# Kernel tuning notes

Hardware: AMD Instinct MI355X
Metric: run time of the kernel (lower is better)

Reference implementation:

```python
import jax, jax.numpy as jnp
import numpy as np

N_GROUPS = 32
EPS = 1e-5
N_HEADS = 4
D_K = 64


def group_norm(x, gamma, beta):
    # x: [B, C, H, W]; normalize over (channels within group, spatial)
    B, C, H, W = x.shape
    xg = x.reshape(B, N_GROUPS, C // N_GROUPS, H, W)
    mean = jnp.mean(xg, axis=(2, 3, 4), keepdims=True)
    var = jnp.var(xg, axis=(2, 3, 4), keepdims=True)
    xn = ((xg - mean) * jax.lax.rsqrt(var + EPS)).reshape(B, C, H, W)
    return xn * gamma[None, :, None, None] + beta[None, :, None, None]


def setup_inputs() -> dict:
    key = jax.random.key(0)
    ks = jax.random.split(key, 4)
    B, C, H, W = 4, 256, 64, 64
    x = jax.random.normal(ks[0], (B, C, H, W), dtype=jnp.float32)
    gamma = jnp.ones((C,), dtype=jnp.float32)
    beta = jnp.zeros((C,), dtype=jnp.float32)
    w_qkv = jax.random.normal(ks[1], (C, N_HEADS * D_K * 3), dtype=jnp.float32) * (C ** -0.5)
    b_qkv = jnp.zeros((N_HEADS * D_K * 3,), dtype=jnp.float32)
    w_out = jax.random.normal(ks[2], (N_HEADS * D_K, C), dtype=jnp.float32) * ((N_HEADS * D_K) ** -0.5)
    b_out = jnp.zeros((C,), dtype=jnp.float32)
    return {"x": x, "gamma": gamma, "beta": beta, "w_qkv": w_qkv,
            "b_qkv": b_qkv, "w_out": w_out, "b_out": b_out}


def reference(x, gamma, beta, w_qkv, b_qkv, w_out, b_out):
    B, C, H, W = x.shape
    S = H * W
    scale = D_K ** -0.5
    # GroupNorm -> [B, S, C]
    h = group_norm(x, gamma, beta).reshape(B, C, S).transpose(0, 2, 1)
    qkv = (h @ w_qkv + b_qkv).reshape(B, S, N_HEADS, 3 * D_K)
    q, k, v = jnp.split(qkv, 3, axis=-1)          # each [B, S, H, D]
    attn = jnp.einsum('bihd,bjhd->bijh', q, k) * scale
    attn = jax.nn.softmax(attn, axis=2)           # softmax over j (keys)
    res = jnp.einsum('bijh,bjhd->bihd', attn, v)  # [B, S, H, D]
    res = res.reshape(B, S, N_HEADS * D_K)
    res = res @ w_out + b_out                     # [B, S, C]
    res = res.transpose(0, 2, 1).reshape(B, C, H, W)
    return res + x
```

## Files before the change

kernel.cpp:

```cpp
#include <hip/hip_runtime.h>
#include <hip/hip_bf16.h>


typedef __attribute__((ext_vector_type(8))) short short8;
typedef __attribute__((ext_vector_type(4))) float f32x4;
typedef __attribute__((ext_vector_type(16))) float f32x16;

__device__ __forceinline__ unsigned short f2bf(float f) {
    union { float f; unsigned u; } v; v.f = f;
    unsigned r = v.u + 0x7FFF + ((v.u >> 16) & 1);
    return (unsigned short)(r >> 16);
}

__device__ __forceinline__ unsigned cvt_pk_bf16(float lo, float hi) {
    unsigned r;
    asm("v_cvt_pk_bf16_f32 %0, %1, %2" : "=v"(r) : "v"(lo), "v"(hi));
    return r;
}

__device__ __forceinline__ void permswap(unsigned &x, unsigned &y) {
    asm("v_permlane32_swap_b32 %0, %1" : "+v"(x), "+v"(y));
}

__device__ __forceinline__ float fexp2(float x) {
    float r;
    asm("v_exp_f32 %0, %1" : "=v"(r) : "v"(x));
    return r;
}

__device__ __forceinline__ void gl_lds16(const void* g, void* l) {
    __builtin_amdgcn_global_load_lds(
        (const __attribute__((address_space(1))) void*)(g),
        (__attribute__((address_space(3))) void*)(l), 16, 0, 0);
}

__device__ __forceinline__ f32x16 fzero16() {
    f32x16 z;
    #pragma unroll
    for (int i = 0; i < 16; ++i) z[i] = 0.f;
    return z;
}

__global__ __launch_bounds__(1024) void k_pre(
    const float* __restrict__ x, float* __restrict__ stats,
    const float* __restrict__ wqkv, const float* __restrict__ wout,
    unsigned short* __restrict__ wqkvT, unsigned short* __restrict__ woutT) {
    if (blockIdx.x < 128) {
        int bg = blockIdx.x;
        const float4* xp = (const float4*)(x + bg * 32768);
        float s1 = 0.f, s2 = 0.f;
        for (int i = threadIdx.x; i < 8192; i += 1024) {
            float4 v = xp[i];
            s1 += v.x + v.y + v.z + v.w;
            s2 += v.x*v.x + v.y*v.y + v.z*v.z + v.w*v.w;
        }
        #pragma unroll
        for (int off = 32; off; off >>= 1) {
            s1 += __shfl_down(s1, off);
            s2 += __shfl_down(s2, off);
        }
        __shared__ float r1[16], r2[16];
        int wid = threadIdx.x >> 6;
        if ((threadIdx.x & 63) == 0) { r1[wid] = s1; r2[wid] = s2; }
        __syncthreads();
        if (threadIdx.x == 0) {
            float a = 0.f, b = 0.f;
            #pragma unroll
            for (int i = 0; i < 16; ++i) { a += r1[i]; b += r2[i]; }
            float mean = a * (1.f/32768.f);
            float var  = b * (1.f/32768.f) - mean*mean;
            stats[bg*2]   = mean;
            stats[bg*2+1] = rsqrtf(var + 1e-5f);
        }
    } else {
        int i = (blockIdx.x - 128) * 1024 + threadIdx.x;
        if (i < 196608) {
            int k = i / 768, n = i - k * 768;
            wqkvT[n*256 + k] = f2bf(wqkv[i]);
        }
        if (i < 65536) {
            int k = i >> 8, n = i & 255;
            woutT[n*256 + k] = f2bf(wout[i]);
        }
    }
}

__global__ __launch_bounds__(512, 2) void k_qkvf(
    const float* __restrict__ x, const float* __restrict__ gamma,
    const float* __restrict__ beta, const float* __restrict__ stats,
    const unsigned short* __restrict__ wT, const float* __restrict__ bqkv,
    unsigned short* __restrict__ q, unsigned short* __restrict__ kk,
    unsigned short* __restrict__ vT) {
    __shared__ unsigned short t[64][72];
    __shared__ unsigned short lds_h[64][272];

    int m0 = blockIdx.x * 64;
    int b = m0 >> 12;
    int s0 = m0 & 4095;
    int tid = threadIdx.x;

    #pragma unroll
    for (int cb = 0; cb < 4; ++cb) {
        int c0 = cb * 64;
        #pragma unroll
        for (int k = 0; k < 2; ++k) {
            int u = tid + k * 512;
            int cr = u >> 4;
            int sl = (u & 15) * 4;
            int c = c0 + cr;
            float4 v = *(const float4*)&x[(b*256 + c)*4096 + s0 + sl];
            int sg = (b*32 + (c >> 3)) * 2;
            float mean = stats[sg], rstd = stats[sg+1];
            float sa = rstd * gamma[c];
            float sb = beta[c] - mean * sa;
            ushort4 pk;
            pk.x = f2bf(v.x*sa + sb); pk.y = f2bf(v.y*sa + sb);
            pk.z = f2bf(v.z*sa + sb); pk.w = f2bf(v.w*sa + sb);
            *(ushort4*)&t[cr][sl] = pk;
        }
        __syncthreads();
        int sr = tid >> 3;
        int cc8 = (tid & 7) * 8;
        unsigned rr[4];
        #pragma unroll
        for (int j = 0; j < 4; ++j)
            rr[j] = (unsigned)t[cc8 + 2*j][sr] | ((unsigned)t[cc8 + 2*j + 1][sr] << 16);
        *(uint4*)&lds_h[sr][c0 + cc8] = make_uint4(rr[0], rr[1], rr[2], rr[3]);
        __syncthreads();
    }

    int wid = tid >> 6, lane = tid & 63;
    int g = lane >> 4, li = lane & 15;
    int rg = wid & 3, cg = wid >> 2;
    int rowl = rg * 16 + li;
    f32x4 acc[24];
    #pragma unroll
    for (int nt = 0; nt < 24; ++nt) acc[nt] = (f32x4){0.f,0.f,0.f,0.f};
    #pragma unroll
    for (int kt = 0; kt < 8; ++kt) {
        short8 a = *(const short8*)&lds_h[rowl][kt*32 + g*8];
        #pragma unroll
        for (int nt = 0; nt < 24; ++nt) {
            int n = cg*384 + nt*16 + li;
            short8 bb = *(const short8*)&wT[n*256 + kt*32 + g*8];
            acc[nt] = __builtin_amdgcn_mfma_f32_16x16x32_bf16(a, bb, acc[nt], 0, 0, 0);
        }
    }
    int m0w = m0 + rg * 16;
    int s0w = m0w & 4095;
    #pragma unroll
    for (int nt = 0; nt < 24; ++nt) {
        int ng = cg*384 + nt*16 + li;
        int head = cg*2 + nt/12;
        int ntl = nt % 12;
        int bh = b*4 + head;
        float bias = bqkv[ng];
        int d = (ntl & 3)*16 + li;
        if ((ntl >> 2) == 2) {
            ushort4 pk;
            pk.x = f2bf(acc[nt][0] + bias); pk.y = f2bf(acc[nt][1] + bias);
            pk.z = f2bf(acc[nt][2] + bias); pk.w = f2bf(acc[nt][3] + bias);
            *(ushort4*)&vT[(bh*64 + d)*4096 + s0w + g*4] = pk;
        } else if ((ntl >> 2) == 0) {
            #pragma unroll
            for (int r = 0; r < 4; ++r)
                q[(bh*4096 + s0w + g*4 + r)*64 + d] = f2bf((acc[nt][r] + bias) * 0.1803368801f);
        } else {
            #pragma unroll
            for (int r = 0; r < 4; ++r)
                kk[(bh*4096 + s0w + g*4 + r)*64 + d] = f2bf(acc[nt][r] + bias);
        }
    }
}

__global__ __launch_bounds__(512, 4) void k_attn(
    const unsigned short* __restrict__ q, const unsigned short* __restrict__ kk,
    const unsigned short* __restrict__ vT, unsigned short* __restrict__ ao) {
    __shared__ __align__(16) char smem[65536];

    int n = blockIdx.x;
    int qt = n >> 4;
    int bh = ((n & 7) << 1) | ((n >> 3) & 1);
    int tid = threadIdx.x;
    int wid = tid >> 6, lane = tid & 63;
    int qw = wid & 3, st = wid >> 2;
    int hi = lane >> 5, il = lane & 31;
    int swl = (il & 7) << 4;

    int qbase = qt * 128 + qw * 32;
    int qrow = bh * 4096 + qbase + il;
    short8 bq[4];
    #pragma unroll
    for (int kc = 0; kc < 4; ++kc)
        bq[kc] = *(const short8*)&q[qrow*64 + kc*16 + hi*8];

    short8 ones;
    #pragma unroll
    for (int i = 0; i < 8; ++i) ones[i] = (short)0x3F80;

    unsigned p16  = tid * 16;
    unsigned row0 = p16 >> 7;
    unsigned sw   = (row0 & 7) << 4;
    unsigned ks0  = p16 ^ sw;
    unsigned vc0  = (p16 & 127u) ^ sw;
    const char* kbase = (const char*)kk + (size_t)bh * 524288;
    const char* vbase = (const char*)vT + (size_t)(bh*64 + row0) * 8192;
    unsigned woff = wid * 1024;

#define STAGE_PAIR(d, pair) do {                                             \
    const char* _k0 = kbase + (size_t)(2*(pair)) * 8192;                     \
    size_t _vo = (size_t)(2*(pair)) * 128;                                   \
    gl_lds16(_k0 + ks0,              smem + ((d)*2+0)*8192 + woff);          \
    gl_lds16(_k0 + 8192 + ks0,       smem + ((d)*2+1)*8192 + woff);          \
    gl_lds16(vbase + _vo + vc0,       smem + 32768 + ((d)*2+0)*8192 + woff); \
    gl_lds16(vbase + _vo + 128 + vc0, smem + 32768 + ((d)*2+1)*8192 + woff); \
} while (0)

    f32x16 o0 = fzero16(), o1 = fzero16(), accl = fzero16();
    float m_run = 0.f;

    STAGE_PAIR(0, 0);
    asm volatile("s_waitcnt vmcnt(0)" ::: "memory");
    __builtin_amdgcn_s_barrier();
    asm volatile("" ::: "memory");

    int cur = 0;
    for (int tp = 0; tp < 32; ++tp) {
        if (tp < 31) STAGE_PAIR(cur ^ 1, tp + 1);

        const char* kb = smem + (cur*2 + st) * 8192;
        const char* vb = smem + 32768 + (cur*2 + st) * 8192;

        float nm = -m_run;
        f32x16 p0, p1;
        #pragma unroll
        for (int r = 0; r < 16; ++r) { p0[r] = nm; p1[r] = nm; }
        __builtin_amdgcn_s_setprio(1);
        #pragma unroll
        for (int kc = 0; kc < 4; ++kc) {
            int c = (kc*32 + hi*16) ^ swl;
            short8 ka0 = *(const short8*)(kb + il*128 + c);
            short8 ka1 = *(const short8*)(kb + 4096 + il*128 + c);
            p0 = __builtin_amdgcn_mfma_f32_32x32x16_bf16(ka0, bq[kc], p0, 0, 0, 0);
            p1 = __builtin_amdgcn_mfma_f32_32x32x16_bf16(ka1, bq[kc], p1, 0, 0, 0);
        }
        __builtin_amdgcn_s_setprio(0);

        #pragma unroll
        for (int r = 0; r < 16; ++r) {
            p0[r] = fexp2(p0[r]);
            p1[r] = fexp2(p1[r]);
        }
        float m8[8];
        #pragma unroll
        for (int r = 0; r < 8; ++r)
            m8[r] = fmaxf(fmaxf(p0[2*r], p0[2*r+1]), fmaxf(p1[2*r], p1[2*r+1]));
        float pm = fmaxf(fmaxf(fmaxf(m8[0], m8[1]), fmaxf(m8[2], m8[3])),
                         fmaxf(fmaxf(m8[4], m8[5]), fmaxf(m8[6], m8[7])));
        if (__any(pm > 16.f)) {
            pm = fmaxf(pm, __shfl_xor(pm, 32));
            float fac = 1.f / pm;
            m_run += log2f(pm);
            accl[0] *= fac;
            #pragma unroll
            for (int r = 0; r < 16; ++r) {
                o0[r] *= fac; o1[r] *= fac;
                p0[r] *= fac; p1[r] *= fac;
            }
        }

        __builtin_amdgcn_s_setprio(1);
        #pragma unroll
        for (int jc = 0; jc < 4; ++jc) {
            const int hh = jc & 1;
            float e0, e1, e2, e3, e4, e5, e6, e7;
            if (jc < 2) {
                e0 = p0[hh*8+0]; e1 = p0[hh*8+1]; e2 = p0[hh*8+2]; e3 = p0[hh*8+3];
                e4 = p0[hh*8+4]; e5 = p0[hh*8+5]; e6 = p0[hh*8+6]; e7 = p0[hh*8+7];
            } else {
                e0 = p1[hh*8+0]; e1 = p1[hh*8+1]; e2 = p1[hh*8+2]; e3 = p1[hh*8+3];
                e4 = p1[hh*8+4]; e5 = p1[hh*8+5]; e6 = p1[hh*8+6]; e7 = p1[hh*8+7];
            }
            unsigned a = cvt_pk_bf16(e0, e1);
            unsigned b = cvt_pk_bf16(e2, e3);
            unsigned c = cvt_pk_bf16(e4, e5);
            unsigned d = cvt_pk_bf16(e6, e7);
            permswap(a, c);
            permswap(b, d);
            union { unsigned u[4]; short8 s8; } pb;
            pb.u[0] = a; pb.u[1] = b; pb.u[2] = c; pb.u[3] = d;
            int co = (jc*32 + hi*16) ^ swl;
            short8 va0 = *(const short8*)(vb + il*128 + co);
            short8 va1 = *(const short8*)(vb + 4096 + il*128 + co);
            o0   = __builtin_amdgcn_mfma_f32_32x32x16_bf16(va0, pb.s8, o0, 0, 0, 0);
            o1   = __builtin_amdgcn_mfma_f32_32x32x16_bf16(va1, pb.s8, o1, 0, 0, 0);
            accl = __builtin_amdgcn_mfma_f32_32x32x16_bf16(ones, pb.s8, accl, 0, 0, 0);
        }
        __builtin_amdgcn_s_setprio(0);

        if (tp < 31) asm volatile("s_waitcnt vmcnt(0)" ::: "memory");
        asm volatile("" ::: "memory");
        __builtin_amdgcn_s_barrier();
        asm volatile("" ::: "memory");
        cur ^= 1;
    }
#undef STAGE_PAIR

    float l_loc = accl[0];

    float* red = (float*)smem;
    int slot = ((qw*64 + lane) * 34);
    if (st == 1) {
        #pragma unroll
        for (int r = 0; r < 16; ++r) { red[slot + r] = o0[r]; red[slot + 16 + r] = o1[r]; }
        red[slot + 32] = l_loc;
        red[slot + 33] = m_run;
    }
    __syncthreads();
    if (st == 0) {
        float m1 = red[slot + 33], l1 = red[slot + 32];
        float m = fmaxf(m_run, m1);
        float f0 = fexp2(m_run - m), f1 = fexp2(m1 - m);
        float inv = 1.f / (l_loc * f0 + l1 * f1);
        float a0 = f0 * inv, a1 = f1 * inv;
        int b = bh >> 2, hh = bh & 3;
        int s = qbase + il;
        unsigned short* aop = &ao[((size_t)(b*4096 + s))*256 + hh*64];
        #pragma unroll
        for (int rr = 0; rr < 4; ++rr) {
            ushort4 pk0, pk1;
            pk0.x = f2bf(o0[rr*4+0]*a0 + red[slot + rr*4+0]*a1);
            pk0.y = f2bf(o0[rr*4+1]*a0 + red[slot + rr*4+1]*a1);
            pk0.z = f2bf(o0[rr*4+2]*a0 + red[slot + rr*4+2]*a1);
            pk0.w = f2bf(o0[rr*4+3]*a0 + red[slot + rr*4+3]*a1);
            *(ushort4*)&aop[rr*8 + hi*4] = pk0;
            pk1.x = f2bf(o1[rr*4+0]*a0 + red[slot + 16 + rr*4+0]*a1);
            pk1.y = f2bf(o1[rr*4+1]*a0 + red[slot + 16 + rr*4+1]*a1);
            pk1.z = f2bf(o1[rr*4+2]*a0 + red[slot + 16 + rr*4+2]*a1);
            pk1.w = f2bf(o1[rr*4+3]*a0 + red[slot + 16 + rr*4+3]*a1);
            *(ushort4*)&aop[32 + rr*8 + hi*4] = pk1;
        }
    }
}

__global__ __launch_bounds__(256) void k_out(
    const unsigned short* __restrict__ ao, const unsigned short* __restrict__ wT,
    const float* __restrict__ bout, const float* __restrict__ x,
    float* __restrict__ out) {
    int mt = blockIdx.x;
    int tid = threadIdx.x;
    int wid = tid >> 6, lane = tid & 63;
    int g = lane >> 4, li = lane & 15;
    int rg = wid & 1, ch = wid >> 1;
    int m0 = mt * 32 + rg * 16;
    int row = m0 + li;
    f32x4 acc[8];
    #pragma unroll
    for (int nt = 0; nt < 8; ++nt) acc[nt] = (f32x4){0.f,0.f,0.f,0.f};
    #pragma unroll
    for (int kt = 0; kt < 8; ++kt) {
        short8 a = *(const short8*)&ao[row*256 + kt*32 + g*8];
        #pragma unroll
        for (int nt = 0; nt < 8; ++nt) {
            int nn = ch*128 + nt*16 + li;
            short8 b = *(const short8*)&wT[nn*256 + kt*32 + g*8];
            acc[nt] = __builtin_amdgcn_mfma_f32_16x16x32_bf16(a, b, acc[nt], 0, 0, 0);
        }
    }
    int b = m0 >> 12;
    int s0 = (m0 & 4095) + g*4;
    #pragma unroll
    for (int nt = 0; nt < 8; ++nt) {
        int c = ch*128 + nt*16 + li;
        float bias = bout[c];
        int base = (b*256 + c)*4096 + s0;
        float4 xr = *(const float4*)&x[base];
        float4 ov;
        ov.x = acc[nt][0] + bias + xr.x;
        ov.y = acc[nt][1] + bias + xr.y;
        ov.z = acc[nt][2] + bias + xr.z;
        ov.w = acc[nt][3] + bias + xr.w;
        *(float4*)&out[base] = ov;
    }
}

extern "C" void kernel_launch(void* const* d_in, const int* in_sizes, int n_in,
                              void* d_out, int out_size, void* d_ws, size_t ws_size,
                              hipStream_t stream) {
    (void)in_sizes; (void)n_in; (void)out_size; (void)ws_size;
    const float* x     = (const float*)d_in[0];
    const float* gamma = (const float*)d_in[1];
    const float* beta  = (const float*)d_in[2];
    const float* wqkv  = (const float*)d_in[3];
    const float* bqkv  = (const float*)d_in[4];
    const float* wout  = (const float*)d_in[5];
    const float* bout  = (const float*)d_in[6];
    float* out = (float*)d_out;

    char* ws = (char*)d_ws;
    unsigned short* q     = (unsigned short*)(ws + (8u<<20));
    unsigned short* kk    = (unsigned short*)(ws + (16u<<20));
    unsigned short* vT    = (unsigned short*)(ws + (24u<<20));
    unsigned short* ao    = (unsigned short*)(ws + (32u<<20));
    unsigned short* wqkvT = (unsigned short*)(ws + (40u<<20));
    unsigned short* woutT = (unsigned short*)(ws + (40u<<20) + 393216);
    float*          stats = (float*)(ws + (40u<<20) + 524288);

    k_pre<<<320, 1024, 0, stream>>>(x, stats, wqkv, wout, wqkvT, woutT);
    k_qkvf<<<256, 512, 0, stream>>>(x, gamma, beta, stats, wqkvT, bqkv, q, kk, vT);
    k_attn<<<dim3(512), 512, 0, stream>>>(q, kk, vT, ao);
    k_out<<<dim3(512), 256, 0, stream>>>(ao, woutT, bout, x, out);
}
```

Before: 170.4 us.

## Retile QKV GEMM warps and stage output-projection tile through LDS for coalesced stores

```diff
diff --git a/kernel.cpp b/kernel.cpp
--- a/kernel.cpp
+++ b/kernel.cpp
@@ -131,44 +131,47 @@
 
     int wid = tid >> 6, lane = tid & 63;
     int g = lane >> 4, li = lane & 15;
-    int rg = wid & 3, cg = wid >> 2;
-    int rowl = rg * 16 + li;
-    f32x4 acc[24];
-    #pragma unroll
-    for (int nt = 0; nt < 24; ++nt) acc[nt] = (f32x4){0.f,0.f,0.f,0.f};
+    int rg = wid & 1, cg = wid >> 1;
+    f32x4 acc[2][12];
+    #pragma unroll
+    for (int rt = 0; rt < 2; ++rt)
+        #pragma unroll
+        for (int nt = 0; nt < 12; ++nt) acc[rt][nt] = (f32x4){0.f,0.f,0.f,0.f};
     #pragma unroll
     for (int kt = 0; kt < 8; ++kt) {
-        short8 a = *(const short8*)&lds_h[rowl][kt*32 + g*8];
-        #pragma unroll
-        for (int nt = 0; nt < 24; ++nt) {
-            int n = cg*384 + nt*16 + li;
+        short8 a0 = *(const short8*)&lds_h[rg*32 + li][kt*32 + g*8];
+        short8 a1 = *(const short8*)&lds_h[rg*32 + 16 + li][kt*32 + g*8];
+        #pragma unroll
+        for (int nt = 0; nt < 12; ++nt) {
+            int n = cg*192 + nt*16 + li;
             short8 bb = *(const short8*)&wT[n*256 + kt*32 + g*8];
-            acc[nt] = __builtin_amdgcn_mfma_f32_16x16x32_bf16(a, bb, acc[nt], 0, 0, 0);
-        }
-    }
-    int m0w = m0 + rg * 16;
-    int s0w = m0w & 4095;
-    #pragma unroll
-    for (int nt = 0; nt < 24; ++nt) {
-        int ng = cg*384 + nt*16 + li;
-        int head = cg*2 + nt/12;
-        int ntl = nt % 12;
-        int bh = b*4 + head;
-        float bias = bqkv[ng];
-        int d = (ntl & 3)*16 + li;
-        if ((ntl >> 2) == 2) {
-            ushort4 pk;
-            pk.x = f2bf(acc[nt][0] + bias); pk.y = f2bf(acc[nt][1] + bias);
-            pk.z = f2bf(acc[nt][2] + bias); pk.w = f2bf(acc[nt][3] + bias);
-            *(ushort4*)&vT[(bh*64 + d)*4096 + s0w + g*4] = pk;
-        } else if ((ntl >> 2) == 0) {
-            #pragma unroll
-            for (int r = 0; r < 4; ++r)
-                q[(bh*4096 + s0w + g*4 + r)*64 + d] = f2bf((acc[nt][r] + bias) * 0.1803368801f);
-        } else {
-            #pragma unroll
-            for (int r = 0; r < 4; ++r)
-                kk[(bh*4096 + s0w + g*4 + r)*64 + d] = f2bf(acc[nt][r] + bias);
+            acc[0][nt] = __builtin_amdgcn_mfma_f32_16x16x32_bf16(a0, bb, acc[0][nt], 0, 0, 0);
+            acc[1][nt] = __builtin_amdgcn_mfma_f32_16x16x32_bf16(a1, bb, acc[1][nt], 0, 0, 0);
+        }
+    }
+    int bh = b*4 + cg;
+    #pragma unroll
+    for (int rt = 0; rt < 2; ++rt) {
+        int s0w = s0 + rg*32 + rt*16;
+        #pragma unroll
+        for (int nt = 0; nt < 12; ++nt) {
+            int ng = cg*192 + nt*16 + li;
+            float bias = bqkv[ng];
+            int d = (nt & 3)*16 + li;
+            if ((nt >> 2) == 2) {
+                ushort4 pk;
+                pk.x = f2bf(acc[rt][nt][0] + bias); pk.y = f2bf(acc[rt][nt][1] + bias);
+                pk.z = f2bf(acc[rt][nt][2] + bias); pk.w = f2bf(acc[rt][nt][3] + bias);
+                *(ushort4*)&vT[(bh*64 + d)*4096 + s0w + g*4] = pk;
+            } else if ((nt >> 2) == 0) {
+                #pragma unroll
+                for (int r = 0; r < 4; ++r)
+                    q[(bh*4096 + s0w + g*4 + r)*64 + d] = f2bf((acc[rt][nt][r] + bias) * 0.1803368801f);
+            } else {
+                #pragma unroll
+                for (int r = 0; r < 4; ++r)
+                    kk[(bh*4096 + s0w + g*4 + r)*64 + d] = f2bf(acc[rt][nt][r] + bias);
+            }
         }
     }
 }
@@ -343,17 +346,18 @@
     }
 }
 
-__global__ __launch_bounds__(256) void k_out(
+__global__ __launch_bounds__(512) void k_out(
     const unsigned short* __restrict__ ao, const unsigned short* __restrict__ wT,
     const float* __restrict__ bout, const float* __restrict__ x,
     float* __restrict__ out) {
+    __shared__ float lds_fT[256][68];
     int mt = blockIdx.x;
     int tid = threadIdx.x;
     int wid = tid >> 6, lane = tid & 63;
     int g = lane >> 4, li = lane & 15;
-    int rg = wid & 1, ch = wid >> 1;
-    int m0 = mt * 32 + rg * 16;
-    int row = m0 + li;
+    int rg = wid & 3, ch = wid >> 2;
+    int m0 = mt * 64;
+    int row = m0 + rg*16 + li;
     f32x4 acc[8];
     #pragma unroll
     for (int nt = 0; nt < 8; ++nt) acc[nt] = (f32x4){0.f,0.f,0.f,0.f};
@@ -367,20 +371,26 @@
             acc[nt] = __builtin_amdgcn_mfma_f32_16x16x32_bf16(a, b, acc[nt], 0, 0, 0);
         }
     }
-    int b = m0 >> 12;
-    int s0 = (m0 & 4095) + g*4;
     #pragma unroll
     for (int nt = 0; nt < 8; ++nt) {
         int c = ch*128 + nt*16 + li;
         float bias = bout[c];
-        int base = (b*256 + c)*4096 + s0;
+        #pragma unroll
+        for (int r = 0; r < 4; ++r)
+            lds_fT[c][rg*16 + g*4 + r] = acc[nt][r] + bias;
+    }
+    __syncthreads();
+    int b = m0 >> 12;
+    int s0 = m0 & 4095;
+    #pragma unroll
+    for (int p = 0; p < 8; ++p) {
+        int c = p*32 + (tid >> 4);
+        int sl = (tid & 15) * 4;
+        float4 t = *(const float4*)&lds_fT[c][sl];
+        int base = (b*256 + c)*4096 + s0 + sl;
         float4 xr = *(const float4*)&x[base];
-        float4 ov;
-        ov.x = acc[nt][0] + bias + xr.x;
-        ov.y = acc[nt][1] + bias + xr.y;
-        ov.z = acc[nt][2] + bias + xr.z;
-        ov.w = acc[nt][3] + bias + xr.w;
-        *(float4*)&out[base] = ov;
+        t.x += xr.x; t.y += xr.y; t.z += xr.z; t.w += xr.w;
+        *(float4*)&out[base] = t;
     }
 }
 
@@ -409,5 +419,5 @@
     k_pre<<<320, 1024, 0, stream>>>(x, stats, wqkv, wout, wqkvT, woutT);
     k_qkvf<<<256, 512, 0, stream>>>(x, gamma, beta, stats, wqkvT, bqkv, q, kk, vT);
     k_attn<<<dim3(512), 512, 0, stream>>>(q, kk, vT, ao);
-    k_out<<<dim3(512), 256, 0, stream>>>(ao, woutT, bout, x, out);
-}
+    k_out<<<dim3(256), 512, 0, stream>>>(ao, woutT, bout, x, out);
+}
```

New measurement: 150.6 us (median of 3 runs). 11.6% less time.
